# Optimization experiments

Hardware: AMD Instinct MI355X
Metric: run time of the kernel (lower is better)

Reference implementation:

```python
import jax, jax.numpy as jnp
import numpy as np

B, LQ, LK, D, H, DK, DV = 8, 1024, 1024, 512, 8, 64, 64
EPS = 1e-14          # K.epsilon()**2 with default K.epsilon()=1e-7
MASK_VALUE = -1e30   # default mask_value in call()


def setup_inputs() -> dict:
    key = jax.random.key(0)
    ks = jax.random.split(key, 7)
    query = jax.random.normal(ks[0], (B, LQ, D), jnp.float32)
    key_t = jax.random.normal(ks[1], (B, LK, D), jnp.float32)
    value = jax.random.normal(ks[2], (B, LK, D), jnp.float32)
    mask = jax.random.randint(ks[3], (B, LK), 0, 2).astype(jnp.float32)
    glorot = np.sqrt(2.0 / (D + DK)).astype(np.float32)
    Wq = jax.random.normal(ks[4], (H, D, DK), jnp.float32) * glorot
    Wk = jax.random.normal(ks[5], (H, D, DK), jnp.float32) * glorot
    Wv = jax.random.normal(ks[6], (H, D, DV), jnp.float32) * glorot
    gamma = jnp.ones((1,), jnp.float32)
    beta = jnp.zeros((1,), jnp.float32)
    return {"query": query, "key": key_t, "value": value, "mask": mask,
            "Wq": Wq, "Wk": Wk, "Wv": Wv, "gamma": gamma, "beta": beta}


def reference(query, key, value, mask, Wq, Wk, Wv, gamma, beta):
    # Per-head projections (the original's Python loop over heads, vectorized).
    q = jnp.einsum('bqd,hde->bhqe', query, Wq)   # [B,H,LQ,DK]
    k = jnp.einsum('bkd,hde->bhke', key, Wk)     # [B,H,LK,DK]
    v = jnp.einsum('bkd,hde->bhke', value, Wv)   # [B,H,LK,DV]
    # NOTE: no 1/sqrt(dk) scaling, faithful to the source.
    A = jnp.einsum('bhqe,bhke->bhqk', q, k)      # [B,H,LQ,LK]
    m = mask[:, None, None, :]                    # [B,1,1,LK] broadcast over heads & queries
    A = m * A + (1.0 - m) * MASK_VALUE
    A = jax.nn.softmax(A, axis=-1)
    o = jnp.einsum('bhqk,bhke->bhqe', A, v)      # [B,H,LQ,DV]
    conc = o.transpose(0, 2, 1, 3).reshape(B, LQ, H * DV)  # concat heads
    # Scalar-affine layernorm over the concatenated feature dim.
    mean = jnp.mean(conc, axis=-1, keepdims=True)
    var = jnp.mean(jnp.square(conc - mean), axis=-1, keepdims=True)
    x = (conc - mean) / jnp.sqrt(var + EPS)
    return x * gamma[0] + beta[0]
```

## Files before the change

### kernel.cpp

```cpp
#include <hip/hip_runtime.h>
#include <math.h>

#define NB 8
#define NLQ 1024
#define NLK 1024
#define ND 512
#define NH 8
#define MASKV -1e30f
#define LOG2E 1.44269504088896f
#define SHIFT2 32.0f

typedef unsigned short ushort_t;
typedef __attribute__((ext_vector_type(8))) _Float16 f16x8;
typedef __attribute__((ext_vector_type(8))) short bf16x8;
typedef __attribute__((ext_vector_type(16))) float f32x16;

__device__ __forceinline__ ushort_t f2h_bits(float f) {
    union { _Float16 h; ushort_t u; } v; v.h = (_Float16)f;
    return v.u;
}
__device__ __forceinline__ ushort_t f2bf(float f) {
    union { float f; unsigned u; } v; v.f = f;
    unsigned r = v.u + 0x7fffu + ((v.u >> 16) & 1u);
    return (ushort_t)(r >> 16);
}
__device__ __forceinline__ void gload16(const ushort_t* g, ushort_t* l) {
    __builtin_amdgcn_global_load_lds(
        (const __attribute__((address_space(1))) void*)g,
        (__attribute__((address_space(3))) void*)l, 16, 0, 0);
}
__device__ __forceinline__ unsigned pack_bf16_trunc(float p0, float p1) {
    return __builtin_amdgcn_perm(__float_as_uint(p1), __float_as_uint(p0),
                                 0x07060302u);
}
__device__ __forceinline__ unsigned pack_f16(float a, float b) {
    return (unsigned)f2h_bits(a) | ((unsigned)f2h_bits(b) << 16);
}

__global__ __launch_bounds__(256) void wsplit_kernel(
    const float* __restrict__ Wq, const float* __restrict__ Wk, const float* __restrict__ Wv,
    ushort_t* __restrict__ oq, ushort_t* __restrict__ ok, ushort_t* __restrict__ ov) {
    __shared__ float T[64][65];
    const int d0 = blockIdx.x * 64;
    const int h  = blockIdx.y;
    const int t  = blockIdx.z;
    const float* W = (t == 0) ? Wq : (t == 1) ? Wk : Wv;
    ushort_t* oh = (t == 0) ? oq : (t == 1) ? ok : ov;
    const int tid = threadIdx.x;
#pragma unroll
    for (int i = 0; i < 4; i++) {
        int r = (tid >> 4) + i * 16;
        int c = (tid & 15) * 4;
        float4 v = *(const float4*)&W[((size_t)h * ND + d0 + r) * 64 + c];
        *(float4*)&T[r][c] = v;
    }
    __syncthreads();
    const int e = tid & 63;
    const int dg = tid >> 6;
    ushort_t hs[16];
#pragma unroll
    for (int dd = 0; dd < 16; dd++) hs[dd] = f2h_bits(T[dg * 16 + dd][e]);
    size_t base = ((size_t)h * 64 + e) * ND + d0 + dg * 16;
#pragma unroll
    for (int c = 0; c < 2; c++) {
        uint4 wh;
        wh.x = (unsigned)hs[8*c+0] | ((unsigned)hs[8*c+1] << 16);
        wh.y = (unsigned)hs[8*c+2] | ((unsigned)hs[8*c+3] << 16);
        wh.z = (unsigned)hs[8*c+4] | ((unsigned)hs[8*c+5] << 16);
        wh.w = (unsigned)hs[8*c+6] | ((unsigned)hs[8*c+7] << 16);
        *(uint4*)&oh[base + 8 * c] = wh;
    }
}

__global__ __launch_bounds__(256, 4) void proj_mfma_kernel(
    const float* __restrict__ Xq, const float* __restrict__ Xk,
    const float* __restrict__ Xv, const ushort_t* __restrict__ Wbase,
    ushort_t* __restrict__ Obase) {
    __shared__ ushort_t sX[2][4160];
    __shared__ ushort_t sW[2][4160];

    const int l0 = blockIdx.x * 64;
    const int h  = blockIdx.y;
    const int z  = blockIdx.z;
    const int t  = z >> 3;
    const int b  = z & 7;
    const int tid  = threadIdx.x;
    const int wave = tid >> 6;
    const int lane = tid & 63;
    const int l31  = lane & 31;
    const int hib  = lane >> 5;
    const size_t bh = (size_t)b * NH + h;

    const float* Xt = (t == 0) ? Xq : (t == 1) ? Xk : Xv;
    const float* gx = Xt + ((size_t)b * NLQ + l0) * ND;
    const ushort_t* gw = Wbase + (size_t)t * ((size_t)NH * 64 * ND)
                       + (size_t)h * 64 * ND;
    ushort_t* out = Obase + (size_t)t * ((size_t)NB * NH * NLQ * 64);

    const int srow = lane >> 3;
    const int schk = (lane & 7) ^ srow;
    const int dslot = srow * 64 + (lane & 7) * 8;

    auto stage_w = [&](int buf, int d0) {
#pragma unroll
        for (int i = 0; i < 2; i++) {
            int u = i * 4 + wave;
            int row = u * 8 + srow;
            gload16(gw + (size_t)row * ND + d0 + schk * 8, sW[buf] + u * 520);
        }
    };
    auto load_x = [&](int d0, float4* xa, float4* xb) {
#pragma unroll
        for (int i = 0; i < 2; i++) {
            int u = i * 4 + wave;
            int row = u * 8 + srow;
            const float* src = gx + (size_t)row * ND + d0 + schk * 8;
            xa[i] = *(const float4*)src;
            xb[i] = *(const float4*)(src + 4);
        }
    };
    auto write_x = [&](int buf, const float4* xa, const float4* xb) {
#pragma unroll
        for (int i = 0; i < 2; i++) {
            int u = i * 4 + wave;
            uint4 w;
            w.x = pack_f16(xa[i].x, xa[i].y);
            w.y = pack_f16(xa[i].z, xa[i].w);
            w.z = pack_f16(xb[i].x, xb[i].y);
            w.w = pack_f16(xb[i].z, xb[i].w);
            *(uint4*)&sX[buf][u * 520 + dslot] = w;
        }
    };

    f32x16 acc;
#pragma unroll
    for (int i = 0; i < 16; i++) acc[i] = 0.f;

    const int arow = (wave >> 1) * 32 + l31;
    const int brow = (wave & 1) * 32 + l31;
    const int apad = (arow >> 3) * 520 + (arow & 7) * 64;
    const int bpad = (brow >> 3) * 520 + (brow & 7) * 64;
    const int sw = l31 & 7;

    {
        float4 xa[2], xb[2];
        load_x(0, xa, xb);
        stage_w(0, 0);
        write_x(0, xa, xb);
    }
    __syncthreads();
    int cur = 0;
    for (int kc = 0; kc < 8; kc++) {
        float4 xa[2], xb[2];
        if (kc < 7) {
            load_x((kc + 1) * 64, xa, xb);
            stage_w(cur ^ 1, (kc + 1) * 64);
        }
#pragma unroll
        for (int c = 0; c < 4; c++) {
            const int pc = ((2 * c + hib) ^ sw) * 8;
            f16x8 xh = *(const f16x8*)&sX[cur][apad + pc];
            f16x8 wh = *(const f16x8*)&sW[cur][bpad + pc];
            acc = __builtin_amdgcn_mfma_f32_32x32x16_f16(xh, wh, acc, 0, 0, 0);
        }
        if (kc < 7) write_x(cur ^ 1, xa, xb);
        __syncthreads();
        cur ^= 1;
    }

    if (t < 2) {
        const float scale = (t == 0) ? LOG2E : 1.f;
        const size_t obase = (bh * NLQ + l0) * 64;
        const int e = (wave & 1) * 32 + l31;
#pragma unroll
        for (int r = 0; r < 16; r++) {
            int l = (wave >> 1) * 32 + (r & 3) + 8 * (r >> 2) + 4 * hib;
            out[obase + (size_t)l * 64 + e] = f2h_bits(acc[r] * scale);
        }
    } else {
        ushort_t (*T)[68] = (ushort_t(*)[68])sX;
        const int e = (wave & 1) * 32 + l31;
#pragma unroll
        for (int r = 0; r < 16; r++) {
            int l = (wave >> 1) * 32 + (r & 3) + 8 * (r >> 2) + 4 * hib;
            T[e][l] = f2bf(acc[r]);
        }
        __syncthreads();
        const int e2 = tid >> 2;
        const int lc = (tid & 3) * 16;
        size_t base = (bh * 64 + e2) * NLK + l0 + lc;
        *(uint4*)&out[base]     = *(const uint4*)&T[e2][lc];
        *(uint4*)&out[base + 8] = *(const uint4*)&T[e2][lc + 8];
    }
}

__global__ __launch_bounds__(256, 4) void attn_kernel(
    const ushort_t* __restrict__ Qf, const ushort_t* __restrict__ Kf,
    const ushort_t* __restrict__ Vt, const float* __restrict__ maskp,
    float* __restrict__ Op) {
    __shared__ ushort_t sK[2][4160];
    __shared__ ushort_t sV[2][4160];
    __shared__ float sBias[1024];

    const int idx = blockIdx.x;
    const int bh_i = idx & 63;
    const int qc  = idx >> 6;
    const int b = bh_i >> 3, h = bh_i & 7;
    const size_t bh = (size_t)b * NH + h;

    const int tid  = threadIdx.x;
    const int wave = tid >> 6;
    const int lane = tid & 63;
    const int l31  = lane & 31;
    const int hib  = lane >> 5;
    const int q = qc * 128 + wave * 32 + l31;
    const int sw = l31 & 7;

    {
        const float* mrow = maskp + ((size_t)b << 10);
        float4 m0 = *(const float4*)&mrow[tid * 4];
        float4 bi;
        bi.x = (m0.x > 0.5f) ? -SHIFT2 : MASKV;
        bi.y = (m0.y > 0.5f) ? -SHIFT2 : MASKV;
        bi.z = (m0.z > 0.5f) ? -SHIFT2 : MASKV;
        bi.w = (m0.w > 0.5f) ? -SHIFT2 : MASKV;
        *(float4*)&sBias[tid * 4] = bi;
    }

    f16x8 qh[4];
    {
        const ushort_t* ph = Qf + (bh * NLQ + q) * 64 + hib * 8;
#pragma unroll
        for (int c = 0; c < 4; c++) qh[c] = *(const f16x8*)(ph + c * 16);
    }

    const int srow = lane >> 3;
    const int schk = (lane & 7) ^ srow;

    auto stage = [&](int buf, int k0) {
#pragma unroll
        for (int n = 0; n < 4; n++) {
            int u = wave + n * 4;
            if (u < 8) {
                int row = u * 8 + srow;
                int key = (row & ~12) | ((row & 4) << 1) | ((row & 8) >> 1);
                gload16(Kf + ((bh << 10) + k0 + key) * 64 + schk * 8,
                        sK[buf] + u * 520);
            } else {
                int u8 = u - 8;
                int row = u8 * 8 + srow;
                gload16(Vt + ((bh << 6) + row) * NLK + k0 + schk * 8,
                        sV[buf] + u8 * 520);
            }
        }
    };

    f32x16 O0, O1;
#pragma unroll
    for (int i = 0; i < 16; i++) { O0[i] = 0.f; O1[i] = 0.f; }
    float lrun = 0.f;

    const int rp0 = (l31 >> 3) * 520 + (l31 & 7) * 64;
    const int rp1 = rp0 + 4 * 520;

    stage(0, 0);
    __syncthreads();
    int cur = 0;

    for (int t = 0; t < 16; t++) {
        const int k0 = t << 6;
        if (t < 15) stage(cur ^ 1, k0 + 64);

        f32x16 S0, S1;
#pragma unroll
        for (int g = 0; g < 4; g++) {
            const int kb = k0 + 16 * (g >> 1) + 8 * hib + 4 * (g & 1);
            float4 b0 = *(const float4*)&sBias[kb];
            float4 b1 = *(const float4*)&sBias[kb + 32];
            S0[4 * g + 0] = b0.x; S0[4 * g + 1] = b0.y;
            S0[4 * g + 2] = b0.z; S0[4 * g + 3] = b0.w;
            S1[4 * g + 0] = b1.x; S1[4 * g + 1] = b1.y;
            S1[4 * g + 2] = b1.z; S1[4 * g + 3] = b1.w;
        }
#pragma unroll
        for (int c = 0; c < 4; c++) {
            const int pc = ((2 * c + hib) ^ sw) * 8;
            f16x8 a0 = *(const f16x8*)&sK[cur][rp0 + pc];
            f16x8 a1 = *(const f16x8*)&sK[cur][rp1 + pc];
            S0 = __builtin_amdgcn_mfma_f32_32x32x16_f16(a0, qh[c], S0, 0, 0, 0);
            S1 = __builtin_amdgcn_mfma_f32_32x32x16_f16(a1, qh[c], S1, 0, 0, 0);
        }

        unsigned pq[8][2];
#pragma unroll
        for (int g = 0; g < 8; g++) {
            float p0, p1, p2, p3;
            if (g < 4) {
                p0 = __builtin_amdgcn_exp2f(S0[4*g+0]);
                p1 = __builtin_amdgcn_exp2f(S0[4*g+1]);
                p2 = __builtin_amdgcn_exp2f(S0[4*g+2]);
                p3 = __builtin_amdgcn_exp2f(S0[4*g+3]);
            } else {
                p0 = __builtin_amdgcn_exp2f(S1[4*(g-4)+0]);
                p1 = __builtin_amdgcn_exp2f(S1[4*(g-4)+1]);
                p2 = __builtin_amdgcn_exp2f(S1[4*(g-4)+2]);
                p3 = __builtin_amdgcn_exp2f(S1[4*(g-4)+3]);
            }
            lrun += (p0 + p1) + (p2 + p3);
            pq[g][0] = pack_bf16_trunc(p0, p1);
            pq[g][1] = pack_bf16_trunc(p2, p3);
        }

#pragma unroll
        for (int c = 0; c < 4; c++) {
            union { unsigned u[4]; bf16x8 v; } pf;
            pf.u[0] = pq[2 * c][0];     pf.u[1] = pq[2 * c][1];
            pf.u[2] = pq[2 * c + 1][0]; pf.u[3] = pq[2 * c + 1][1];
            const int pc = ((2 * c + hib) ^ sw) * 8;
            bf16x8 v0 = *(const bf16x8*)&sV[cur][rp0 + pc];
            bf16x8 v1 = *(const bf16x8*)&sV[cur][rp1 + pc];
            O0 = __builtin_amdgcn_mfma_f32_32x32x16_bf16(v0, pf.v, O0, 0, 0, 0);
            O1 = __builtin_amdgcn_mfma_f32_32x32x16_bf16(v1, pf.v, O1, 0, 0, 0);
        }
        __syncthreads();
        cur ^= 1;
    }

    lrun += __shfl_xor(lrun, 32);
    const float linv = 1.f / lrun;
    float* obase = Op + ((size_t)(b * NLQ + q)) * (NH * 64) + h * 64;
#pragma unroll
    for (int me = 0; me < 2; me++) {
#pragma unroll
        for (int g = 0; g < 4; g++) {
            int e0 = me * 32 + 8 * g + 4 * hib;
            float4 o;
            if (me == 0) {
                o.x = O0[4 * g + 0] * linv; o.y = O0[4 * g + 1] * linv;
                o.z = O0[4 * g + 2] * linv; o.w = O0[4 * g + 3] * linv;
            } else {
                o.x = O1[4 * g + 0] * linv; o.y = O1[4 * g + 1] * linv;
                o.z = O1[4 * g + 2] * linv; o.w = O1[4 * g + 3] * linv;
            }
            *(float4*)&obase[e0] = o;
        }
    }
}

__global__ __launch_bounds__(256) void ln_kernel(const float* __restrict__ X,
                                                 const float* __restrict__ gamma,
                                                 const float* __restrict__ beta,
                                                 float* __restrict__ out) {
    const int row = blockIdx.x * 4 + (threadIdx.x >> 6);
    const int lane = threadIdx.x & 63;
    const float* x = &X[(size_t)row * 512];
    float4 v0 = *(const float4*)&x[lane * 8];
    float4 v1 = *(const float4*)&x[lane * 8 + 4];
    float sum = v0.x + v0.y + v0.z + v0.w + v1.x + v1.y + v1.z + v1.w;
    float sq = v0.x * v0.x + v0.y * v0.y + v0.z * v0.z + v0.w * v0.w
             + v1.x * v1.x + v1.y * v1.y + v1.z * v1.z + v1.w * v1.w;
#pragma unroll
    for (int off = 32; off > 0; off >>= 1) {
        sum += __shfl_down(sum, off);
        sq  += __shfl_down(sq, off);
    }
    sum = __shfl(sum, 0);
    sq  = __shfl(sq, 0);
    const float mean = sum * (1.f / 512.f);
    const float var = sq * (1.f / 512.f) - mean * mean;
    const float rstd = rsqrtf(var + 1e-14f);
    const float g = gamma[0], be = beta[0];
    float* o = &out[(size_t)row * 512];
    float4 r0, r1;
    r0.x = (v0.x - mean) * rstd * g + be;  r0.y = (v0.y - mean) * rstd * g + be;
    r0.z = (v0.z - mean) * rstd * g + be;  r0.w = (v0.w - mean) * rstd * g + be;
    r1.x = (v1.x - mean) * rstd * g + be;  r1.y = (v1.y - mean) * rstd * g + be;
    r1.z = (v1.z - mean) * rstd * g + be;  r1.w = (v1.w - mean) * rstd * g + be;
    *(float4*)&o[lane * 8] = r0;
    *(float4*)&o[lane * 8 + 4] = r1;
}

extern "C" void kernel_launch(void* const* d_in, const int* in_sizes, int n_in,
                              void* d_out, int out_size, void* d_ws, size_t ws_size,
                              hipStream_t stream) {
    const float* query = (const float*)d_in[0];
    const float* key_t = (const float*)d_in[1];
    const float* value = (const float*)d_in[2];
    const float* mask  = (const float*)d_in[3];
    const float* Wq    = (const float*)d_in[4];
    const float* Wk    = (const float*)d_in[5];
    const float* Wv    = (const float*)d_in[6];
    const float* gamma = (const float*)d_in[7];
    const float* beta  = (const float*)d_in[8];
    float* out = (float*)d_out;

    const size_t A = (size_t)NB * NLQ * ND;
    const size_t WS = (size_t)NH * 64 * ND;
    ushort_t* Qf = (ushort_t*)d_ws;
    ushort_t* Kf = Qf + A;
    ushort_t* Vt = Qf + 2 * A;
    ushort_t* Wt = Qf + 3 * A;

    wsplit_kernel<<<dim3(ND / 64, NH, 3), 256, 0, stream>>>(
        Wq, Wk, Wv, Wt, Wt + WS, Wt + 2 * WS);

    proj_mfma_kernel<<<dim3(NLQ / 64, NH, 24), 256, 0, stream>>>(
        query, key_t, value, Wt, Qf);

    attn_kernel<<<512, 256, 0, stream>>>(Qf, Kf, Vt, mask, out);

    ln_kernel<<<(NB * NLQ) / 4, 256, 0, stream>>>(out, gamma, beta, out);
}
```

Measured before the change: 170.1 us.

## Enlarge projection tile to 128 rows with two accumulators per wave

```diff
diff --git a/kernel.cpp b/kernel.cpp
--- a/kernel.cpp
+++ b/kernel.cpp
@@ -35,6 +35,9 @@
 }
 __device__ __forceinline__ unsigned pack_f16(float a, float b) {
     return (unsigned)f2h_bits(a) | ((unsigned)f2h_bits(b) << 16);
+}
+__device__ __forceinline__ unsigned pack_bf16_rne(float a, float b) {
+    return (unsigned)f2bf(a) | ((unsigned)f2bf(b) << 16);
 }
 
 __global__ __launch_bounds__(256) void wsplit_kernel(
@@ -46,6 +49,7 @@
     const int t  = blockIdx.z;
     const float* W = (t == 0) ? Wq : (t == 1) ? Wk : Wv;
     ushort_t* oh = (t == 0) ? oq : (t == 1) ? ok : ov;
+    const float scale = (t == 0) ? LOG2E : 1.f;
     const int tid = threadIdx.x;
 #pragma unroll
     for (int i = 0; i < 4; i++) {
@@ -59,7 +63,7 @@
     const int dg = tid >> 6;
     ushort_t hs[16];
 #pragma unroll
-    for (int dd = 0; dd < 16; dd++) hs[dd] = f2h_bits(T[dg * 16 + dd][e]);
+    for (int dd = 0; dd < 16; dd++) hs[dd] = f2h_bits(T[dg * 16 + dd][e] * scale);
     size_t base = ((size_t)h * 64 + e) * ND + d0 + dg * 16;
 #pragma unroll
     for (int c = 0; c < 2; c++) {
@@ -72,14 +76,14 @@
     }
 }
 
-__global__ __launch_bounds__(256, 4) void proj_mfma_kernel(
+__global__ __launch_bounds__(256, 3) void proj_mfma_kernel(
     const float* __restrict__ Xq, const float* __restrict__ Xk,
     const float* __restrict__ Xv, const ushort_t* __restrict__ Wbase,
     ushort_t* __restrict__ Obase) {
-    __shared__ ushort_t sX[2][4160];
-    __shared__ ushort_t sW[2][4160];
-
-    const int l0 = blockIdx.x * 64;
+    __shared__ ushort_t sX[2][16 * 520];
+    __shared__ ushort_t sW[2][8 * 520];
+
+    const int lb = blockIdx.x * 128;
     const int h  = blockIdx.y;
     const int z  = blockIdx.z;
     const int t  = z >> 3;
@@ -89,10 +93,12 @@
     const int lane = tid & 63;
     const int l31  = lane & 31;
     const int hib  = lane >> 5;
+    const int lhalf = wave & 1;
+    const int ehalf = wave >> 1;
     const size_t bh = (size_t)b * NH + h;
 
     const float* Xt = (t == 0) ? Xq : (t == 1) ? Xk : Xv;
-    const float* gx = Xt + ((size_t)b * NLQ + l0) * ND;
+    const float* gx = Xt + ((size_t)b * NLQ + lb) * ND;
     const ushort_t* gw = Wbase + (size_t)t * ((size_t)NH * 64 * ND)
                        + (size_t)h * 64 * ND;
     ushort_t* out = Obase + (size_t)t * ((size_t)NB * NH * NLQ * 64);
@@ -111,7 +117,7 @@
     };
     auto load_x = [&](int d0, float4* xa, float4* xb) {
 #pragma unroll
-        for (int i = 0; i < 2; i++) {
+        for (int i = 0; i < 4; i++) {
             int u = i * 4 + wave;
             int row = u * 8 + srow;
             const float* src = gx + (size_t)row * ND + d0 + schk * 8;
@@ -121,7 +127,7 @@
     };
     auto write_x = [&](int buf, const float4* xa, const float4* xb) {
 #pragma unroll
-        for (int i = 0; i < 2; i++) {
+        for (int i = 0; i < 4; i++) {
             int u = i * 4 + wave;
             uint4 w;
             w.x = pack_f16(xa[i].x, xa[i].y);
@@ -132,18 +138,19 @@
         }
     };
 
-    f32x16 acc;
-#pragma unroll
-    for (int i = 0; i < 16; i++) acc[i] = 0.f;
-
-    const int arow = (wave >> 1) * 32 + l31;
-    const int brow = (wave & 1) * 32 + l31;
-    const int apad = (arow >> 3) * 520 + (arow & 7) * 64;
-    const int bpad = (brow >> 3) * 520 + (brow & 7) * 64;
+    f32x16 acc0, acc1;
+#pragma unroll
+    for (int i = 0; i < 16; i++) { acc0[i] = 0.f; acc1[i] = 0.f; }
+
+    const int arow0 = lhalf * 64 + l31;
+    const int apad0 = (arow0 >> 3) * 520 + (arow0 & 7) * 64;
+    const int apad1 = apad0 + 4 * 520;
+    const int brow  = ehalf * 32 + l31;
+    const int bpad  = (brow >> 3) * 520 + (brow & 7) * 64;
     const int sw = l31 & 7;
 
     {
-        float4 xa[2], xb[2];
+        float4 xa[4], xb[4];
         load_x(0, xa, xb);
         stage_w(0, 0);
         write_x(0, xa, xb);
@@ -151,7 +158,7 @@
     __syncthreads();
     int cur = 0;
     for (int kc = 0; kc < 8; kc++) {
-        float4 xa[2], xb[2];
+        float4 xa[4], xb[4];
         if (kc < 7) {
             load_x((kc + 1) * 64, xa, xb);
             stage_w(cur ^ 1, (kc + 1) * 64);
@@ -159,9 +166,11 @@
 #pragma unroll
         for (int c = 0; c < 4; c++) {
             const int pc = ((2 * c + hib) ^ sw) * 8;
-            f16x8 xh = *(const f16x8*)&sX[cur][apad + pc];
-            f16x8 wh = *(const f16x8*)&sW[cur][bpad + pc];
-            acc = __builtin_amdgcn_mfma_f32_32x32x16_f16(xh, wh, acc, 0, 0, 0);
+            f16x8 a0 = *(const f16x8*)&sX[cur][apad0 + pc];
+            f16x8 a1 = *(const f16x8*)&sX[cur][apad1 + pc];
+            f16x8 wv = *(const f16x8*)&sW[cur][bpad + pc];
+            acc0 = __builtin_amdgcn_mfma_f32_32x32x16_f16(a0, wv, acc0, 0, 0, 0);
+            acc1 = __builtin_amdgcn_mfma_f32_32x32x16_f16(a1, wv, acc1, 0, 0, 0);
         }
         if (kc < 7) write_x(cur ^ 1, xa, xb);
         __syncthreads();
@@ -169,28 +178,35 @@
     }
 
     if (t < 2) {
-        const float scale = (t == 0) ? LOG2E : 1.f;
-        const size_t obase = (bh * NLQ + l0) * 64;
-        const int e = (wave & 1) * 32 + l31;
+        const size_t ob = (bh * NLQ + lb + lhalf * 64) * 64;
+        const int e = ehalf * 32 + l31;
 #pragma unroll
         for (int r = 0; r < 16; r++) {
-            int l = (wave >> 1) * 32 + (r & 3) + 8 * (r >> 2) + 4 * hib;
-            out[obase + (size_t)l * 64 + e] = f2h_bits(acc[r] * scale);
+            int lr = (r & 3) + 8 * (r >> 2) + 4 * hib;
+            out[ob + (size_t)lr * 64 + e]        = f2h_bits(acc0[r]);
+            out[ob + (size_t)(32 + lr) * 64 + e] = f2h_bits(acc1[r]);
         }
     } else {
-        ushort_t (*T)[68] = (ushort_t(*)[68])sX;
-        const int e = (wave & 1) * 32 + l31;
-#pragma unroll
-        for (int r = 0; r < 16; r++) {
-            int l = (wave >> 1) * 32 + (r & 3) + 8 * (r >> 2) + 4 * hib;
-            T[e][l] = f2bf(acc[r]);
+        ushort_t (*T)[136] = (ushort_t(*)[136])sX;
+        const int e = ehalf * 32 + l31;
+#pragma unroll
+        for (int g = 0; g < 4; g++) {
+            int lr = lhalf * 64 + 8 * g + 4 * hib;
+            uint2 w0, w1;
+            w0.x = pack_bf16_rne(acc0[4 * g + 0], acc0[4 * g + 1]);
+            w0.y = pack_bf16_rne(acc0[4 * g + 2], acc0[4 * g + 3]);
+            w1.x = pack_bf16_rne(acc1[4 * g + 0], acc1[4 * g + 1]);
+            w1.y = pack_bf16_rne(acc1[4 * g + 2], acc1[4 * g + 3]);
+            *(uint2*)&T[e][lr]      = w0;
+            *(uint2*)&T[e][lr + 32] = w1;
         }
         __syncthreads();
         const int e2 = tid >> 2;
-        const int lc = (tid & 3) * 16;
-        size_t base = (bh * 64 + e2) * NLK + l0 + lc;
-        *(uint4*)&out[base]     = *(const uint4*)&T[e2][lc];
-        *(uint4*)&out[base + 8] = *(const uint4*)&T[e2][lc + 8];
+        const int lc = (tid & 3) * 32;
+        size_t basev = (bh * 64 + e2) * NLK + lb + lc;
+#pragma unroll
+        for (int c4 = 0; c4 < 4; c4++)
+            *(uint4*)&out[basev + c4 * 8] = *(const uint4*)&T[e2][lc + c4 * 8];
     }
 }
 
@@ -404,7 +420,7 @@
     wsplit_kernel<<<dim3(ND / 64, NH, 3), 256, 0, stream>>>(
         Wq, Wk, Wv, Wt, Wt + WS, Wt + 2 * WS);
 
-    proj_mfma_kernel<<<dim3(NLQ / 64, NH, 24), 256, 0, stream>>>(
+    proj_mfma_kernel<<<dim3(NLQ / 128, NH, 24), 256, 0, stream>>>(
         query, key_t, value, Wt, Qf);
 
     attn_kernel<<<512, 256, 0, stream>>>(Qf, Kf, Vt, mask, out);
```

Result: no change. 171.1 us (+0.6%).
